# Kernel optimization log

Measured on AMD Instinct MI355X. Metric: run time of the kernel, lower is better.

Reference implementation:

```python
import jax, jax.numpy as jnp
import numpy as np

B, S, E, H = 4, 1024, 1024, 16
HD = E // H

def setup_inputs() -> dict:
    key = jax.random.key(0)
    ks = jax.random.split(key, 12)
    std = 1.0 / np.sqrt(E)
    inp = {
        "query": jax.random.normal(ks[0], (B, S, E), jnp.float32),
        "key_t": jax.random.normal(ks[1], (B, S, E), jnp.float32),
        "value": jax.random.normal(ks[2], (B, S, E), jnp.float32),
        # causal mask, broadcastable to (B, H, S, S); 0 => masked
        "mask": jnp.tril(jnp.ones((S, S), jnp.int32))[None, None],
        "Wq": jax.random.normal(ks[3], (E, E), jnp.float32) * std,
        "bq": jnp.zeros((E,), jnp.float32),
        "Wk": jax.random.normal(ks[4], (E, E), jnp.float32) * std,
        "bk": jnp.zeros((E,), jnp.float32),
        "Wv": jax.random.normal(ks[5], (E, E), jnp.float32) * std,
        "bv": jnp.zeros((E,), jnp.float32),
        "Wo": jax.random.normal(ks[6], (E, E), jnp.float32) * std,
        "bo": jnp.zeros((E,), jnp.float32),
    }
    return inp

def reference(query, key_t, value, mask, Wq, bq, Wk, bk, Wv, bv, Wo, bo):
    scale = jnp.asarray(np.sqrt(HD), query.dtype)
    # projections (torch Linear: x @ W.T + b), split into heads -> (B, H, S, HD)
    def split_heads(x):
        return x.reshape(B, S, H, HD).transpose(0, 2, 1, 3)
    q = split_heads(query @ Wq.T + bq)
    k = split_heads(key_t @ Wk.T + bk)
    v = split_heads(value @ Wv.T + bv)
    scores = jnp.einsum("bhqd,bhkd->bhqk", q, k) / scale  # (B,H,S,S)
    scores = jnp.where(mask == 0, jnp.asarray(-jnp.inf, scores.dtype), scores)
    attn = jax.nn.softmax(scores, axis=-1)
    # dropout is identity in eval / p=0
    out = jnp.einsum("bhqk,bhkd->bhqd", attn, v)
    out = out.transpose(0, 2, 1, 3).reshape(B, S, E)
    out = out @ Wo.T + bo
    return out, attn
```

## Files before the change

kernel.cpp:

```cpp
#include <hip/hip_runtime.h>
#include <hip/hip_bf16.h>


typedef short bf16x8 __attribute__((ext_vector_type(8)));
typedef float f32x4 __attribute__((ext_vector_type(4)));

#define VMCNT(n) asm volatile("s_waitcnt vmcnt(" #n ")" ::: "memory")

__device__ __forceinline__ unsigned short f2bf(float f) {
  union { float f; unsigned u; } v; v.f = f;
  unsigned r = v.u + 0x7FFF + ((v.u >> 16) & 1);
  return (unsigned short)(r >> 16);
}

__device__ __forceinline__ float bf2f(unsigned short u) {
  union { unsigned u; float f; } v; v.u = ((unsigned)u) << 16;
  return v.f;
}

__device__ __forceinline__ void gload16(const unsigned short* g, unsigned short* l) {
  __builtin_amdgcn_global_load_lds(
      (const __attribute__((address_space(1))) unsigned int*)g,
      (__attribute__((address_space(3))) unsigned int*)l, 16, 0, 0);
}

__global__ __launch_bounds__(256) void cast3_k(
    const float* __restrict__ a, const float* __restrict__ b,
    const float* __restrict__ c,
    unsigned short* __restrict__ oa, unsigned short* __restrict__ ob,
    unsigned short* __restrict__ oc) {
  const float* in = blockIdx.y == 0 ? a : blockIdx.y == 1 ? b : c;
  unsigned short* out = blockIdx.y == 0 ? oa : blockIdx.y == 1 ? ob : oc;
  int i = (blockIdx.x * 256 + threadIdx.x) * 8;
  float4 x = *(const float4*)(in + i);
  float4 y = *(const float4*)(in + i + 4);
  unsigned short t[8] = { f2bf(x.x), f2bf(x.y), f2bf(x.z), f2bf(x.w),
                          f2bf(y.x), f2bf(y.y), f2bf(y.z), f2bf(y.w) };
  *(bf16x8*)(out + i) = *(bf16x8*)t;
}

__global__ __launch_bounds__(256) void cast4_k(
    const float* __restrict__ a, const float* __restrict__ b,
    const float* __restrict__ c, const float* __restrict__ d,
    unsigned short* __restrict__ oa, unsigned short* __restrict__ ob,
    unsigned short* __restrict__ oc, unsigned short* __restrict__ od) {
  const float* in = blockIdx.y == 0 ? a : blockIdx.y == 1 ? b : blockIdx.y == 2 ? c : d;
  unsigned short* out = blockIdx.y == 0 ? oa : blockIdx.y == 1 ? ob : blockIdx.y == 2 ? oc : od;
  int i = (blockIdx.x * 256 + threadIdx.x) * 8;
  float4 x = *(const float4*)(in + i);
  float4 y = *(const float4*)(in + i + 4);
  unsigned short t[8] = { f2bf(x.x), f2bf(x.y), f2bf(x.z), f2bf(x.w),
                          f2bf(y.x), f2bf(y.y), f2bf(y.z), f2bf(y.w) };
  *(bf16x8*)(out + i) = *(bf16x8*)t;
}

__device__ __forceinline__ void gemm_core(
    const unsigned short* __restrict__ A, const unsigned short* __restrict__ W,
    int m0, int n0, int K, unsigned short* As, unsigned short* Bs, f32x4 acc[4][4])
{
  const int tid = threadIdx.x;
  const int w = tid >> 6, lane = tid & 63, quad = lane >> 4, lc = lane & 15;
  const int wm = (w >> 1) * 64, wn = (w & 1) * 64;
  const int lrow = lane >> 3, lg = lane & 7;

  for (int kb = 0; kb < K; kb += 64) {
#pragma unroll
    for (int t = 0; t < 4; t++) {
      int row = w * 32 + t * 8 + lrow;
      int gsw = lg ^ (row & 7);
      gload16(&A[(size_t)(m0 + row) * K + kb + gsw * 8], &As[(w * 32 + t * 8) * 64]);
      gload16(&W[(size_t)(n0 + row) * K + kb + gsw * 8], &Bs[(w * 32 + t * 8) * 64]);
    }
    __syncthreads();
#pragma unroll
    for (int kk = 0; kk < 2; kk++) {
      bf16x8 af[4], bfr[4];
#pragma unroll
      for (int i = 0; i < 4; i++) {
        int ra = wm + i * 16 + lc;
        af[i] = *(const bf16x8*)&As[ra * 64 + (((kk * 4 + quad) ^ (ra & 7)) * 8)];
      }
#pragma unroll
      for (int j = 0; j < 4; j++) {
        int rb = wn + j * 16 + lc;
        bfr[j] = *(const bf16x8*)&Bs[rb * 64 + (((kk * 4 + quad) ^ (rb & 7)) * 8)];
      }
#pragma unroll
      for (int i = 0; i < 4; i++)
#pragma unroll
        for (int j = 0; j < 4; j++)
          acc[i][j] = __builtin_amdgcn_mfma_f32_16x16x32_bf16(af[i], bfr[j], acc[i][j], 0, 0, 0);
    }
    __syncthreads();
  }
}

__global__ __launch_bounds__(256) void gemm_qkv(
    const unsigned short* __restrict__ Xq, const unsigned short* __restrict__ Xk,
    const unsigned short* __restrict__ Xv,
    const unsigned short* __restrict__ Wq, const unsigned short* __restrict__ Wk,
    const unsigned short* __restrict__ Wv,
    const float* __restrict__ bq, const float* __restrict__ bk, const float* __restrict__ bv,
    unsigned short* __restrict__ Qb, unsigned short* __restrict__ Kb,
    unsigned short* __restrict__ Vt)
{
  __shared__ __align__(16) unsigned short S[128 * 136];
  unsigned short* As = S;
  unsigned short* Bs = S + 128 * 64;
  const int z = blockIdx.z;
  const unsigned short* A = z == 0 ? Xq : z == 1 ? Xk : Xv;
  const unsigned short* W = z == 0 ? Wq : z == 1 ? Wk : Wv;
  const float* bias = z == 0 ? bq : z == 1 ? bk : bv;
  unsigned short* outRM = z == 0 ? Qb : Kb;
  const int m0 = blockIdx.x * 128, n0 = blockIdx.y * 128;
  const int tid = threadIdx.x;
  const int w = tid >> 6, lane = tid & 63, quad = lane >> 4, lc = lane & 15;
  const int wm = (w >> 1) * 64, wn = (w & 1) * 64;

  f32x4 acc[4][4] = {};
  gemm_core(A, W, m0, n0, 1024, As, Bs, acc);

  if (z < 2) {
#pragma unroll
    for (int j = 0; j < 4; j++) {
      int col = n0 + wn + j * 16 + lc;
      float bvl = bias[col];
#pragma unroll
      for (int i = 0; i < 4; i++)
#pragma unroll
        for (int r = 0; r < 4; r++) {
          int row = m0 + wm + i * 16 + quad * 4 + r;
          outRM[(size_t)row * 1024 + col] = f2bf(acc[i][j][r] + bvl);
        }
    }
  } else {
    unsigned short* T = S;
#pragma unroll
    for (int j = 0; j < 4; j++) {
      int col = wn + j * 16 + lc;
      float bvl = bias[n0 + col];
#pragma unroll
      for (int i = 0; i < 4; i++)
#pragma unroll
        for (int r = 0; r < 4; r++) {
          int row = wm + i * 16 + quad * 4 + r;
          T[col * 136 + (((row >> 3) ^ (col & 7)) << 3) + (row & 7)] =
              f2bf(acc[i][j][r] + bvl);
        }
    }
    __syncthreads();
    const int b_ = m0 >> 10, sb = m0 & 1023;
#pragma unroll
    for (int it = 0; it < 8; it++) {
      int cl = w * 32 + it * 4 + (lane >> 4);
      int sg = lane & 15;
      int colg = n0 + cl;
      *(bf16x8*)&Vt[((size_t)((b_ * 16 + (colg >> 6)) * 64 + (colg & 63))) * 1024 + sb + sg * 8] =
          *(const bf16x8*)&T[cl * 136 + ((sg ^ (cl & 7)) << 3)];
    }
  }
}

__global__ __launch_bounds__(256) void gemm_out(
    const unsigned short* __restrict__ A, const unsigned short* __restrict__ W,
    const float* __restrict__ bias, float* __restrict__ outf)
{
  __shared__ __align__(16) unsigned short As[128 * 64];
  __shared__ __align__(16) unsigned short Bs[128 * 64];
  const int m0 = blockIdx.x * 128, n0 = blockIdx.y * 128;
  const int tid = threadIdx.x;
  const int w = tid >> 6, lane = tid & 63, quad = lane >> 4, lc = lane & 15;
  const int wm = (w >> 1) * 64, wn = (w & 1) * 64;

  f32x4 acc[4][4] = {};
  gemm_core(A, W, m0, n0, 1024, As, Bs, acc);

#pragma unroll
  for (int j = 0; j < 4; j++) {
    int col = n0 + wn + j * 16 + lc;
    float bvl = bias[col];
#pragma unroll
    for (int i = 0; i < 4; i++)
#pragma unroll
      for (int r = 0; r < 4; r++) {
        int row = m0 + wm + i * 16 + quad * 4 + r;
        outf[(size_t)row * 1024 + col] = acc[i][j][r] + bvl;
      }
  }
}

__global__ __launch_bounds__(256) void attn_fused(
    const unsigned short* __restrict__ Qb,
    const unsigned short* __restrict__ Kb,
    const unsigned short* __restrict__ Vt,
    float* __restrict__ attn,
    unsigned short* __restrict__ O)
{
  __shared__ __align__(16) unsigned short Ks[2][64 * 64];
  __shared__ __align__(16) unsigned short Vs[2][64 * 64];
  __shared__ __align__(16) unsigned short Pl[4][16][40];
  const int bh = blockIdx.x, b = bh >> 4, h = bh & 15;
  const int by = (int)gridDim.y - 1 - (int)blockIdx.y;
  const int q0 = by * 64;
  const int tid = threadIdx.x;
  const int w = tid >> 6, lane = tid & 63, quad = lane >> 4, lc = lane & 15;
  const int g0 = q0 + w * 16;
  const int kt_d = g0 >> 4;
  const int nch = by + 1;
  const int sr = lane >> 3, sg = lane & 7;
  const int r0_ = w * 8 + sr, r1_ = 32 + r0_;

  bf16x8 a0, a1;
  {
    const unsigned short* qp = Qb + ((size_t)(b * 1024 + g0 + lc)) * 1024 + h * 64 + quad * 8;
    bf16x8 q0v = *(const bf16x8*)qp;
    bf16x8 q1v = *(const bf16x8*)(qp + 32);
#pragma unroll
    for (int i = 0; i < 8; i++) {
      a0[i] = (short)f2bf(bf2f((unsigned short)q0v[i]) * 0.125f);
      a1[i] = (short)f2bf(bf2f((unsigned short)q1v[i]) * 0.125f);
    }
  }

  float m_[4] = { -1e30f, -1e30f, -1e30f, -1e30f };
  float l_[4] = { 0.f, 0.f, 0.f, 0.f };

  {
    gload16(&Kb[((size_t)(b * 1024 + 0 + r0_)) * 1024 + h * 64 + (sg ^ (r0_ & 7)) * 8],
            &Ks[0][(w * 8) * 64]);
    gload16(&Kb[((size_t)(b * 1024 + 0 + r1_)) * 1024 + h * 64 + (sg ^ (r1_ & 7)) * 8],
            &Ks[0][(32 + w * 8) * 64]);
  }
  for (int c = 0; c < nch; c++) {
    const unsigned short* Kc = Ks[c & 1];
    int kv0 = c * 64;
    if (c + 1 < nch) {
      int nv0 = kv0 + 64;
      unsigned short* Kn = Ks[(c + 1) & 1];
      gload16(&Kb[((size_t)(b * 1024 + nv0 + r0_)) * 1024 + h * 64 + (sg ^ (r0_ & 7)) * 8],
              &Kn[(w * 8) * 64]);
      gload16(&Kb[((size_t)(b * 1024 + nv0 + r1_)) * 1024 + h * 64 + (sg ^ (r1_ & 7)) * 8],
              &Kn[(32 + w * 8) * 64]);
      VMCNT(2);
    } else {
      VMCNT(0);
    }
    __builtin_amdgcn_s_barrier();
    __builtin_amdgcn_sched_barrier(0);
    int tmax = kt_d - c * 4;
    int tlim = tmax < 3 ? tmax : 3;
    for (int t = 0; t <= tlim; t++) {
      int rk = t * 16 + lc;
      const unsigned short* kr = &Kc[rk * 64];
      bf16x8 b0 = *(const bf16x8*)&kr[((quad ^ (rk & 7))) * 8];
      bf16x8 b1 = *(const bf16x8*)&kr[(((quad + 4) ^ (rk & 7))) * 8];
      f32x4 c0 = {}, c1 = {};
      c0 = __builtin_amdgcn_mfma_f32_16x16x32_bf16(a0, b0, c0, 0, 0, 0);
      c1 = __builtin_amdgcn_mfma_f32_16x16x32_bf16(a1, b1, c1, 0, 0, 0);
      if (t < tmax) {
#pragma unroll
        for (int r = 0; r < 4; r++) {
          float s = c0[r] + c1[r];
          float mn = fmaxf(m_[r], s);
          l_[r] = l_[r] * __expf(m_[r] - mn) + __expf(s - mn);
          m_[r] = mn;
        }
      } else {
#pragma unroll
        for (int r = 0; r < 4; r++) {
          int qr = g0 + quad * 4 + r;
          float sv = (kv0 + t * 16 + lc) > qr ? -1e30f : c0[r] + c1[r];
          float mn = fmaxf(m_[r], sv);
          l_[r] = l_[r] * __expf(m_[r] - mn) + __expf(sv - mn);
          m_[r] = mn;
        }
      }
    }
    asm volatile("s_waitcnt lgkmcnt(0)" ::: "memory");
    __builtin_amdgcn_s_barrier();
    __builtin_amdgcn_sched_barrier(0);
  }

  float mofs[4];
#pragma unroll
  for (int r = 0; r < 4; r++) {
    float mT = m_[r];
#pragma unroll
    for (int off = 1; off < 16; off <<= 1) mT = fmaxf(mT, __shfl_xor(mT, off));
    float lt = l_[r] * __expf(m_[r] - mT);
#pragma unroll
    for (int off = 1; off < 16; off <<= 1) lt += __shfl_xor(lt, off);
    mofs[r] = mT + __logf(lt);
  }

  float* arow = attn + (size_t)bh * 1024 * 1024;
  f32x4 oacc[4] = {};
  {
    gload16(&Kb[((size_t)(b * 1024 + 0 + r0_)) * 1024 + h * 64 + (sg ^ (r0_ & 7)) * 8],
            &Ks[0][(w * 8) * 64]);
    gload16(&Kb[((size_t)(b * 1024 + 0 + r1_)) * 1024 + h * 64 + (sg ^ (r1_ & 7)) * 8],
            &Ks[0][(32 + w * 8) * 64]);
    gload16(&Vt[((size_t)(bh * 64 + r0_)) * 1024 + 0 + (sg ^ (r0_ & 7)) * 8],
            &Vs[0][(w * 8) * 64]);
    gload16(&Vt[((size_t)(bh * 64 + r1_)) * 1024 + 0 + (sg ^ (r1_ & 7)) * 8],
            &Vs[0][(32 + w * 8) * 64]);
  }
  for (int c = 0; c < nch; c++) {
    const unsigned short* Kc = Ks[c & 1];
    const unsigned short* Vc = Vs[c & 1];
    int kv0 = c * 64;
    if (c + 1 < nch) {
      int nv0 = kv0 + 64;
      unsigned short* Kn = Ks[(c + 1) & 1];
      unsigned short* Vn = Vs[(c + 1) & 1];
      gload16(&Kb[((size_t)(b * 1024 + nv0 + r0_)) * 1024 + h * 64 + (sg ^ (r0_ & 7)) * 8],
              &Kn[(w * 8) * 64]);
      gload16(&Kb[((size_t)(b * 1024 + nv0 + r1_)) * 1024 + h * 64 + (sg ^ (r1_ & 7)) * 8],
              &Kn[(32 + w * 8) * 64]);
      gload16(&Vt[((size_t)(bh * 64 + r0_)) * 1024 + nv0 + (sg ^ (r0_ & 7)) * 8],
              &Vn[(w * 8) * 64]);
      gload16(&Vt[((size_t)(bh * 64 + r1_)) * 1024 + nv0 + (sg ^ (r1_ & 7)) * 8],
              &Vn[(32 + w * 8) * 64]);
      VMCNT(4);
    } else {
      VMCNT(0);
    }
    __builtin_amdgcn_s_barrier();
    __builtin_amdgcn_sched_barrier(0);
    int tmax = kt_d - c * 4;
#pragma unroll
    for (int u = 0; u < 2; u++) {
      if (u * 2 <= tmax) {
#pragma unroll
        for (int t2 = 0; t2 < 2; t2++) {
          int t = u * 2 + t2;
          if (t <= tmax) {
            int rk = t * 16 + lc;
            const unsigned short* kr = &Kc[rk * 64];
            bf16x8 b0 = *(const bf16x8*)&kr[((quad ^ (rk & 7))) * 8];
            bf16x8 b1 = *(const bf16x8*)&kr[(((quad + 4) ^ (rk & 7))) * 8];
            f32x4 c0 = {}, c1 = {};
            c0 = __builtin_amdgcn_mfma_f32_16x16x32_bf16(a0, b0, c0, 0, 0, 0);
            c1 = __builtin_amdgcn_mfma_f32_16x16x32_bf16(a1, b1, c1, 0, 0, 0);
#pragma unroll
            for (int r = 0; r < 4; r++) {
              int qr = g0 + quad * 4 + r;
              float p = (kv0 + t * 16 + lc) > qr ? 0.f
                        : __expf(c0[r] + c1[r] - mofs[r]);
              Pl[w][quad * 4 + r][t2 * 16 + lc] = f2bf(p);
            }
          } else {
#pragma unroll
            for (int r = 0; r < 4; r++) Pl[w][quad * 4 + r][t2 * 16 + lc] = 0;
          }
        }
        {
          int srow = lane >> 2, c4 = lane & 3;
          bf16x8 pv8 = *(const bf16x8*)&Pl[w][srow][c4 * 8];
          float4 f0, f1;
          f0.x = bf2f((unsigned short)pv8[0]); f0.y = bf2f((unsigned short)pv8[1]);
          f0.z = bf2f((unsigned short)pv8[2]); f0.w = bf2f((unsigned short)pv8[3]);
          f1.x = bf2f((unsigned short)pv8[4]); f1.y = bf2f((unsigned short)pv8[5]);
          f1.z = bf2f((unsigned short)pv8[6]); f1.w = bf2f((unsigned short)pv8[7]);
          float* dst = &arow[(size_t)(g0 + srow) * 1024 + kv0 + u * 32 + c4 * 8];
          *(float4*)dst = f0;
          *(float4*)(dst + 4) = f1;
        }
        bf16x8 pa = *(const bf16x8*)&Pl[w][lc][quad * 8];
#pragma unroll
        for (int j = 0; j < 4; j++) {
          int hd = j * 16 + lc;
          bf16x8 bv = *(const bf16x8*)&Vc[hd * 64 + (((u * 4 + quad) ^ (hd & 7)) * 8)];
          oacc[j] = __builtin_amdgcn_mfma_f32_16x16x32_bf16(pa, bv, oacc[j], 0, 0, 0);
        }
      }
    }
    asm volatile("s_waitcnt lgkmcnt(0)" ::: "memory");
    __builtin_amdgcn_s_barrier();
    __builtin_amdgcn_sched_barrier(0);
  }

  {
    int rr = lane >> 2, cl = lane & 3;
    float4 z = make_float4(0.f, 0.f, 0.f, 0.f);
    for (int c0 = g0 + 16 + cl * 4; c0 < 1024; c0 += 16)
      *(float4*)&arow[(size_t)(g0 + rr) * 1024 + c0] = z;
  }

  {
    unsigned short* ob = &Ks[0][0] + w * 1152;
#pragma unroll
    for (int j = 0; j < 4; j++)
#pragma unroll
      for (int r = 0; r < 4; r++)
        ob[(quad * 4 + r) * 72 + j * 16 + lc] = f2bf(oacc[j][r]);
#pragma unroll
    for (int it = 0; it < 2; it++) {
      int row = it * 8 + (lane >> 3), off = (lane & 7) * 8;
      *(bf16x8*)&O[((size_t)(b * 1024 + g0 + row)) * 1024 + h * 64 + off] =
          *(const bf16x8*)&ob[row * 72 + off];
    }
  }
}

extern "C" void kernel_launch(void* const* d_in, const int* in_sizes, int n_in,
                              void* d_out, int out_size, void* d_ws, size_t ws_size,
                              hipStream_t stream) {
  const float* query = (const float*)d_in[0];
  const float* key_t = (const float*)d_in[1];
  const float* value = (const float*)d_in[2];
  const float* Wq = (const float*)d_in[4];
  const float* bq = (const float*)d_in[5];
  const float* Wk = (const float*)d_in[6];
  const float* bk = (const float*)d_in[7];
  const float* Wv = (const float*)d_in[8];
  const float* bv = (const float*)d_in[9];
  const float* Wo = (const float*)d_in[10];
  const float* bo = (const float*)d_in[11];

  unsigned short* Xq  = (unsigned short*)d_ws;
  unsigned short* Xk  = Xq  + 4194304;
  unsigned short* Xv  = Xk  + 4194304;
  unsigned short* Wqb = Xv  + 4194304;
  unsigned short* Wkb = Wqb + 1048576;
  unsigned short* Wvb = Wkb + 1048576;
  unsigned short* Wob = Wvb + 1048576;
  unsigned short* Qb  = Wob + 1048576;
  unsigned short* Kb  = Qb  + 4194304;
  unsigned short* Vtb = Kb  + 4194304;
  unsigned short* Ob  = Vtb + 4194304;

  float* outO = (float*)d_out;
  float* attn = outO + 4194304;

  cast3_k<<<dim3(2048, 3), 256, 0, stream>>>(query, key_t, value, Xq, Xk, Xv);
  cast4_k<<<dim3(512, 4), 256, 0, stream>>>(Wq, Wk, Wv, Wo, Wqb, Wkb, Wvb, Wob);

  gemm_qkv<<<dim3(32, 8, 3), 256, 0, stream>>>(Xq, Xk, Xv, Wqb, Wkb, Wvb,
                                               bq, bk, bv, Qb, Kb, Vtb);

  attn_fused<<<dim3(64, 16), 256, 0, stream>>>(Qb, Kb, Vtb, attn, Ob);

  gemm_out<<<dim3(32, 8), 256, 0, stream>>>(Ob, Wob, bo, outO);
}
```

Baseline: 484.3 us.

## Restructure attention pipeline: single barrier per chunk, batched softmax, nontemporal attn stores

Reworks the fused attention kernel's per-chunk synchronisation so each K/V chunk has one wait-plus-barrier at the top, with the vmcnt wait accounting for the outstanding attn-matrix stores. The stats pass now batches all four score MFMAs before a single online-softmax update per row, which cuts exp and max work. It also adds s_setprio around the MFMA groups, nontemporal stores for the large fp32 attention output, launch bounds with an occupancy hint, and a reordered block-to-query-tile mapping that interleaves heavy and light causal tiles. The goal is to reduce barrier stalls and cache pollution from the write-heavy attn output. The risks are register pressure under the occupancy bound and subtle vmcnt miscounting.

```diff
diff --git a/kernel.cpp b/kernel.cpp
--- a/kernel.cpp
+++ b/kernel.cpp
@@ -189,7 +189,7 @@
   }
 }
 
-__global__ __launch_bounds__(256) void attn_fused(
+__global__ __launch_bounds__(256, 4) void attn_fused(
     const unsigned short* __restrict__ Qb,
     const unsigned short* __restrict__ Kb,
     const unsigned short* __restrict__ Vt,
@@ -200,7 +200,8 @@
   __shared__ __align__(16) unsigned short Vs[2][64 * 64];
   __shared__ __align__(16) unsigned short Pl[4][16][40];
   const int bh = blockIdx.x, b = bh >> 4, h = bh & 15;
-  const int by = (int)gridDim.y - 1 - (int)blockIdx.y;
+  const int yy = (int)blockIdx.y, coh = yy >> 2, pos = yy & 3;
+  const int by = (coh & 1) ? (((coh >> 1) << 2) + pos) : (15 - ((coh >> 1) << 2) - pos);
   const int q0 = by * 64;
   const int tid = threadIdx.x;
   const int w = tid >> 6, lane = tid & 63, quad = lane >> 4, lc = lane & 15;
@@ -225,15 +226,16 @@
   float m_[4] = { -1e30f, -1e30f, -1e30f, -1e30f };
   float l_[4] = { 0.f, 0.f, 0.f, 0.f };
 
-  {
-    gload16(&Kb[((size_t)(b * 1024 + 0 + r0_)) * 1024 + h * 64 + (sg ^ (r0_ & 7)) * 8],
-            &Ks[0][(w * 8) * 64]);
-    gload16(&Kb[((size_t)(b * 1024 + 0 + r1_)) * 1024 + h * 64 + (sg ^ (r1_ & 7)) * 8],
-            &Ks[0][(32 + w * 8) * 64]);
-  }
+  gload16(&Kb[((size_t)(b * 1024 + r0_)) * 1024 + h * 64 + (sg ^ (r0_ & 7)) * 8],
+          &Ks[0][(w * 8) * 64]);
+  gload16(&Kb[((size_t)(b * 1024 + r1_)) * 1024 + h * 64 + (sg ^ (r1_ & 7)) * 8],
+          &Ks[0][(32 + w * 8) * 64]);
   for (int c = 0; c < nch; c++) {
     const unsigned short* Kc = Ks[c & 1];
     int kv0 = c * 64;
+    VMCNT(0);
+    __builtin_amdgcn_s_barrier();
+    __builtin_amdgcn_sched_barrier(0);
     if (c + 1 < nch) {
       int nv0 = kv0 + 64;
       unsigned short* Kn = Ks[(c + 1) & 1];
@@ -241,44 +243,45 @@
               &Kn[(w * 8) * 64]);
       gload16(&Kb[((size_t)(b * 1024 + nv0 + r1_)) * 1024 + h * 64 + (sg ^ (r1_ & 7)) * 8],
               &Kn[(32 + w * 8) * 64]);
-      VMCNT(2);
-    } else {
-      VMCNT(0);
-    }
-    __builtin_amdgcn_s_barrier();
-    __builtin_amdgcn_sched_barrier(0);
+    }
     int tmax = kt_d - c * 4;
     int tlim = tmax < 3 ? tmax : 3;
-    for (int t = 0; t <= tlim; t++) {
-      int rk = t * 16 + lc;
-      const unsigned short* kr = &Kc[rk * 64];
-      bf16x8 b0 = *(const bf16x8*)&kr[((quad ^ (rk & 7))) * 8];
-      bf16x8 b1 = *(const bf16x8*)&kr[(((quad + 4) ^ (rk & 7))) * 8];
-      f32x4 c0 = {}, c1 = {};
-      c0 = __builtin_amdgcn_mfma_f32_16x16x32_bf16(a0, b0, c0, 0, 0, 0);
-      c1 = __builtin_amdgcn_mfma_f32_16x16x32_bf16(a1, b1, c1, 0, 0, 0);
-      if (t < tmax) {
-#pragma unroll
-        for (int r = 0; r < 4; r++) {
-          float s = c0[r] + c1[r];
-          float mn = fmaxf(m_[r], s);
-          l_[r] = l_[r] * __expf(m_[r] - mn) + __expf(s - mn);
-          m_[r] = mn;
-        }
-      } else {
-#pragma unroll
-        for (int r = 0; r < 4; r++) {
-          int qr = g0 + quad * 4 + r;
-          float sv = (kv0 + t * 16 + lc) > qr ? -1e30f : c0[r] + c1[r];
-          float mn = fmaxf(m_[r], sv);
-          l_[r] = l_[r] * __expf(m_[r] - mn) + __expf(sv - mn);
-          m_[r] = mn;
-        }
-      }
-    }
-    asm volatile("s_waitcnt lgkmcnt(0)" ::: "memory");
-    __builtin_amdgcn_s_barrier();
-    __builtin_amdgcn_sched_barrier(0);
+    f32x4 sc[4];
+    __builtin_amdgcn_s_setprio(1);
+#pragma unroll
+    for (int t = 0; t < 4; t++) {
+      if (t <= tlim) {
+        int rk = t * 16 + lc;
+        const unsigned short* kr = &Kc[rk * 64];
+        bf16x8 b0 = *(const bf16x8*)&kr[((quad ^ (rk & 7))) * 8];
+        bf16x8 b1 = *(const bf16x8*)&kr[(((quad + 4) ^ (rk & 7))) * 8];
+        f32x4 c0 = {}, c1 = {};
+        c0 = __builtin_amdgcn_mfma_f32_16x16x32_bf16(a0, b0, c0, 0, 0, 0);
+        c1 = __builtin_amdgcn_mfma_f32_16x16x32_bf16(a1, b1, c1, 0, 0, 0);
+        sc[t] = c0 + c1;
+      }
+    }
+    __builtin_amdgcn_s_setprio(0);
+#pragma unroll
+    for (int r = 0; r < 4; r++) {
+      int qr = g0 + quad * 4 + r;
+      float mc = m_[r];
+      float sv[4];
+#pragma unroll
+      for (int t = 0; t < 4; t++) {
+        if (t <= tlim) {
+          float s = sc[t][r];
+          sv[t] = (t == tmax && (kv0 + t * 16 + lc) > qr) ? -1e30f : s;
+          mc = fmaxf(mc, sv[t]);
+        }
+      }
+      float l = l_[r] * __expf(m_[r] - mc);
+#pragma unroll
+      for (int t = 0; t < 4; t++) {
+        if (t <= tlim) l += __expf(sv[t] - mc);
+      }
+      m_[r] = mc; l_[r] = l;
+    }
   }
 
   float mofs[4];
@@ -293,22 +296,29 @@
     mofs[r] = mT + __logf(lt);
   }
 
+  __builtin_amdgcn_s_barrier();
+  __builtin_amdgcn_sched_barrier(0);
+
   float* arow = attn + (size_t)bh * 1024 * 1024;
   f32x4 oacc[4] = {};
-  {
-    gload16(&Kb[((size_t)(b * 1024 + 0 + r0_)) * 1024 + h * 64 + (sg ^ (r0_ & 7)) * 8],
-            &Ks[0][(w * 8) * 64]);
-    gload16(&Kb[((size_t)(b * 1024 + 0 + r1_)) * 1024 + h * 64 + (sg ^ (r1_ & 7)) * 8],
-            &Ks[0][(32 + w * 8) * 64]);
-    gload16(&Vt[((size_t)(bh * 64 + r0_)) * 1024 + 0 + (sg ^ (r0_ & 7)) * 8],
-            &Vs[0][(w * 8) * 64]);
-    gload16(&Vt[((size_t)(bh * 64 + r1_)) * 1024 + 0 + (sg ^ (r1_ & 7)) * 8],
-            &Vs[0][(32 + w * 8) * 64]);
-  }
+  gload16(&Kb[((size_t)(b * 1024 + r0_)) * 1024 + h * 64 + (sg ^ (r0_ & 7)) * 8],
+          &Ks[0][(w * 8) * 64]);
+  gload16(&Kb[((size_t)(b * 1024 + r1_)) * 1024 + h * 64 + (sg ^ (r1_ & 7)) * 8],
+          &Ks[0][(32 + w * 8) * 64]);
+  gload16(&Vt[((size_t)(bh * 64 + r0_)) * 1024 + (sg ^ (r0_ & 7)) * 8],
+          &Vs[0][(w * 8) * 64]);
+  gload16(&Vt[((size_t)(bh * 64 + r1_)) * 1024 + (sg ^ (r1_ & 7)) * 8],
+          &Vs[0][(32 + w * 8) * 64]);
+  int prevStores = 0;
   for (int c = 0; c < nch; c++) {
     const unsigned short* Kc = Ks[c & 1];
     const unsigned short* Vc = Vs[c & 1];
     int kv0 = c * 64;
+    if (prevStores == 4) { VMCNT(4); }
+    else if (prevStores == 2) { VMCNT(2); }
+    else { VMCNT(0); }
+    __builtin_amdgcn_s_barrier();
+    __builtin_amdgcn_sched_barrier(0);
     if (c + 1 < nch) {
       int nv0 = kv0 + 64;
       unsigned short* Kn = Ks[(c + 1) & 1];
@@ -321,20 +331,19 @@
               &Vn[(w * 8) * 64]);
       gload16(&Vt[((size_t)(bh * 64 + r1_)) * 1024 + nv0 + (sg ^ (r1_ & 7)) * 8],
               &Vn[(32 + w * 8) * 64]);
-      VMCNT(4);
-    } else {
-      VMCNT(0);
-    }
-    __builtin_amdgcn_s_barrier();
+    }
     __builtin_amdgcn_sched_barrier(0);
     int tmax = kt_d - c * 4;
 #pragma unroll
     for (int u = 0; u < 2; u++) {
       if (u * 2 <= tmax) {
+        int nt2 = (u * 2 + 1 <= tmax) ? 2 : 1;
+        f32x4 s2[2];
+        __builtin_amdgcn_s_setprio(1);
 #pragma unroll
         for (int t2 = 0; t2 < 2; t2++) {
-          int t = u * 2 + t2;
-          if (t <= tmax) {
+          if (t2 < nt2) {
+            int t = u * 2 + t2;
             int rk = t * 16 + lc;
             const unsigned short* kr = &Kc[rk * 64];
             bf16x8 b0 = *(const bf16x8*)&kr[((quad ^ (rk & 7))) * 8];
@@ -342,11 +351,18 @@
             f32x4 c0 = {}, c1 = {};
             c0 = __builtin_amdgcn_mfma_f32_16x16x32_bf16(a0, b0, c0, 0, 0, 0);
             c1 = __builtin_amdgcn_mfma_f32_16x16x32_bf16(a1, b1, c1, 0, 0, 0);
+            s2[t2] = c0 + c1;
+          }
+        }
+        __builtin_amdgcn_s_setprio(0);
+#pragma unroll
+        for (int t2 = 0; t2 < 2; t2++) {
+          if (t2 < nt2) {
+            int t = u * 2 + t2;
 #pragma unroll
             for (int r = 0; r < 4; r++) {
               int qr = g0 + quad * 4 + r;
-              float p = (kv0 + t * 16 + lc) > qr ? 0.f
-                        : __expf(c0[r] + c1[r] - mofs[r]);
+              float p = (kv0 + t * 16 + lc) > qr ? 0.f : __expf(s2[t2][r] - mofs[r]);
               Pl[w][quad * 4 + r][t2 * 16 + lc] = f2bf(p);
             }
           } else {
@@ -357,36 +373,37 @@
         {
           int srow = lane >> 2, c4 = lane & 3;
           bf16x8 pv8 = *(const bf16x8*)&Pl[w][srow][c4 * 8];
-          float4 f0, f1;
-          f0.x = bf2f((unsigned short)pv8[0]); f0.y = bf2f((unsigned short)pv8[1]);
-          f0.z = bf2f((unsigned short)pv8[2]); f0.w = bf2f((unsigned short)pv8[3]);
-          f1.x = bf2f((unsigned short)pv8[4]); f1.y = bf2f((unsigned short)pv8[5]);
-          f1.z = bf2f((unsigned short)pv8[6]); f1.w = bf2f((unsigned short)pv8[7]);
+          f32x4 f0, f1;
+          f0[0] = bf2f((unsigned short)pv8[0]); f0[1] = bf2f((unsigned short)pv8[1]);
+          f0[2] = bf2f((unsigned short)pv8[2]); f0[3] = bf2f((unsigned short)pv8[3]);
+          f1[0] = bf2f((unsigned short)pv8[4]); f1[1] = bf2f((unsigned short)pv8[5]);
+          f1[2] = bf2f((unsigned short)pv8[6]); f1[3] = bf2f((unsigned short)pv8[7]);
           float* dst = &arow[(size_t)(g0 + srow) * 1024 + kv0 + u * 32 + c4 * 8];
-          *(float4*)dst = f0;
-          *(float4*)(dst + 4) = f1;
+          __builtin_nontemporal_store(f0, (f32x4*)dst);
+          __builtin_nontemporal_store(f1, (f32x4*)(dst + 4));
         }
         bf16x8 pa = *(const bf16x8*)&Pl[w][lc][quad * 8];
+        __builtin_amdgcn_s_setprio(1);
 #pragma unroll
         for (int j = 0; j < 4; j++) {
           int hd = j * 16 + lc;
           bf16x8 bv = *(const bf16x8*)&Vc[hd * 64 + (((u * 4 + quad) ^ (hd & 7)) * 8)];
           oacc[j] = __builtin_amdgcn_mfma_f32_16x16x32_bf16(pa, bv, oacc[j], 0, 0, 0);
         }
-      }
-    }
-    asm volatile("s_waitcnt lgkmcnt(0)" ::: "memory");
-    __builtin_amdgcn_s_barrier();
-    __builtin_amdgcn_sched_barrier(0);
+        __builtin_amdgcn_s_setprio(0);
+      }
+    }
+    prevStores = (tmax >= 2) ? 4 : 2;
   }
 
   {
     int rr = lane >> 2, cl = lane & 3;
-    float4 z = make_float4(0.f, 0.f, 0.f, 0.f);
+    f32x4 z = { 0.f, 0.f, 0.f, 0.f };
     for (int c0 = g0 + 16 + cl * 4; c0 < 1024; c0 += 16)
-      *(float4*)&arow[(size_t)(g0 + rr) * 1024 + c0] = z;
-  }
-
+      __builtin_nontemporal_store(z, (f32x4*)&arow[(size_t)(g0 + rr) * 1024 + c0]);
+  }
+
+  __syncthreads();
   {
     unsigned short* ob = &Ks[0][0] + w * 1152;
 #pragma unroll
```

Result: slower. 495.9 us (+2.4%).
